# Kernel tuning notes

Measured on AMD Instinct MI355X. Metric: run time of the kernel, lower is better.

The kernel has to match this reference:

```python
import jax, jax.numpy as jnp
import numpy as np

N = 50000      # nodes
E = 500000     # edges per adjacency (avg degree ~10)
IN = 128       # in_dim == hidden_dim so layer weights stack cleanly
HID = 128
C = 40         # n_classes
L = 3          # n_layers
DEG = 10.0


def setup_inputs() -> dict:
    key = jax.random.key(0)
    ks = jax.random.split(key, 14)
    x0 = jax.random.normal(ks[0], (N, IN), jnp.float32)
    # COO sparse adjacency (row-sorted for efficient segment_sum); values mimic mean-normalized weights
    adj_row = jnp.sort(jax.random.randint(ks[1], (E,), 0, N, jnp.int32))
    adj_col = jax.random.randint(ks[2], (E,), 0, N, jnp.int32)
    adj_val = jax.random.uniform(ks[3], (E,), jnp.float32) / DEG
    adj_b_row = jnp.sort(jax.random.randint(ks[4], (E,), 0, N, jnp.int32))
    adj_b_col = jax.random.randint(ks[5], (E,), 0, N, jnp.int32)
    adj_b_val = jax.random.uniform(ks[6], (E,), jnp.float32) / DEG
    id_old_value_new = jax.random.randint(ks[7], (N,), 0, N, jnp.int32)
    mix_ratio = jnp.array([0.5], jnp.float32)
    s = 1.0 / np.sqrt(HID)
    # SAGEConv params: lin_l (applied to aggregated neighbors, carries bias) and lin_r (root)
    Wl = jax.random.uniform(ks[8], (L, HID, HID), jnp.float32, -s, s)
    Wr = jax.random.uniform(ks[9], (L, HID, HID), jnp.float32, -s, s)
    b_sage = jax.random.uniform(ks[10], (L, HID), jnp.float32, -s, s)
    so = 1.0 / np.sqrt(HID)
    W_out = jax.random.uniform(ks[11], (HID, C), jnp.float32, -so, so)
    b_out = jax.random.uniform(ks[12], (C,), jnp.float32, -so, so)
    return dict(x0=x0, adj_row=adj_row, adj_col=adj_col, adj_val=adj_val,
                adj_b_row=adj_b_row, adj_b_col=adj_b_col, adj_b_val=adj_b_val,
                mix_ratio=mix_ratio, id_old_value_new=id_old_value_new,
                Wl=Wl, Wr=Wr, b_sage=b_sage, W_out=W_out, b_out=b_out)


def _sage(x_src, x_dst, row, col, val, Wl_i, Wr_i, b_i):
    # spmm: aggr = adj @ x_src  (gather neighbor feats, scale by edge value, scatter-add to rows)
    msg = x_src[col] * val[:, None]                       # [E, HID]
    aggr = jax.ops.segment_sum(msg, row, num_segments=N)  # [N, HID]
    return aggr @ Wl_i + x_dst @ Wr_i + b_i


def reference(x0, adj_row, adj_col, adj_val, adj_b_row, adj_b_col, adj_b_val,
              mix_ratio, id_old_value_new, Wl, Wr, b_sage, W_out, b_out):
    r = mix_ratio
    # Branch A pre-aggregation stack (dropout is identity in eval mode)
    aggr_xs = [x0]
    x = x0
    for i in range(L - 1):
        x = jax.nn.relu(_sage(x, x, adj_row, adj_col, adj_val, Wl[i], Wr[i], b_sage[i]))
        aggr_xs.append(x)
    # Branch B: gather-based re-indexing of branch-A features
    aggr_xs_b = [h[id_old_value_new] for h in aggr_xs]
    x_mix = aggr_xs[0] * r + aggr_xs_b[0] * (1.0 - r)
    for i in range(L):
        x_new = jax.nn.relu(_sage(aggr_xs[i], x_mix, adj_row, adj_col, adj_val, Wl[i], Wr[i], b_sage[i]))
        x_new_b = jax.nn.relu(_sage(aggr_xs_b[i], x_mix, adj_b_row, adj_b_col, adj_b_val, Wl[i], Wr[i], b_sage[i]))
        x_mix = x_new * r + x_new_b * (1.0 - r)
    logits = x_mix @ W_out + b_out
    return jax.nn.log_softmax(logits, axis=-1)
```

## Files before the change

### kernel.cpp

```cpp
#include <hip/hip_runtime.h>
#include <hip/hip_fp16.h>
#include <math.h>

#define NNODES 50000
#define NEDGES 500000
#define HID 128
#define NCLS 40

using half8v = __attribute__((ext_vector_type(8))) _Float16;
using float4v = __attribute__((ext_vector_type(4))) float;
using uint4v = __attribute__((ext_vector_type(4))) unsigned;

static __device__ __forceinline__ unsigned h2u(__half2 h) {
    union { __half2 h; unsigned u; } x; x.h = h; return x.u;
}
static __device__ __forceinline__ __half2 u2h(unsigned u) {
    union { unsigned u; __half2 h; } x; x.u = u; return x.h;
}

static __device__ __forceinline__ void rowptr_body(const int* __restrict__ row,
                                                   int e, int* __restrict__ rp) {
    if (e >= NEDGES) return;
    int r = row[e];
    int prev = (e == 0) ? -1 : row[e - 1];
    for (int q = prev + 1; q <= r; ++q) rp[q] = e;
    if (e == NEDGES - 1) {
        for (int q = r + 1; q <= NNODES; ++q) rp[q] = NEDGES;
    }
}

static __global__ void prep_edges_kernel(const int* __restrict__ arow,
                                         const int* __restrict__ acol,
                                         const float* __restrict__ aval,
                                         const int* __restrict__ brow,
                                         const int* __restrict__ bcol,
                                         const float* __restrict__ bval,
                                         const int* __restrict__ id,
                                         int* __restrict__ rpa, int* __restrict__ rpb,
                                         int2* __restrict__ cvA, int2* __restrict__ cvB,
                                         int gE) {
    int bid = blockIdx.x;
    if (bid < gE) {
        rowptr_body(arow, bid * 256 + threadIdx.x, rpa);
    } else if (bid < 2 * gE) {
        rowptr_body(brow, (bid - gE) * 256 + threadIdx.x, rpb);
    } else if (bid < 3 * gE) {
        int e = (bid - 2 * gE) * 256 + threadIdx.x;
        if (e < NEDGES) {
            __half2 v = __float2half2_rn(aval[e]);
            cvA[e] = make_int2(acol[e], (int)h2u(v));
        }
    } else {
        int e = (bid - 3 * gE) * 256 + threadIdx.x;
        if (e < NEDGES) {
            __half2 v = __float2half2_rn(bval[e]);
            cvB[e] = make_int2(id[bcol[e]], (int)h2u(v));
        }
    }
}

static __global__ void prep_x_kernel(const float4* __restrict__ x, const int* __restrict__ id,
                                     const float* __restrict__ mixr,
                                     uint2* __restrict__ x0h, uint2* xmh) {
    int i = blockIdx.x * blockDim.x + threadIdx.x;
    int n = i >> 5, qq = i & 31;
    float r = mixr[0];
    float4 a = x[i];
    float4 b = x[(size_t)id[n] * 32 + qq];
    uint2 pa, pm;
    pa.x = h2u(__floats2half2_rn(a.x, a.y));
    pa.y = h2u(__floats2half2_rn(a.z, a.w));
    pm.x = h2u(__floats2half2_rn(r * a.x + (1.f - r) * b.x, r * a.y + (1.f - r) * b.y));
    pm.y = h2u(__floats2half2_rn(r * a.z + (1.f - r) * b.z, r * a.w + (1.f - r) * b.w));
    x0h[i] = pa;
    xmh[i] = pm;
}

static __global__ void prep_w_kernel(const float* __restrict__ Wl, const float* __restrict__ Wr,
                                     const float* __restrict__ Wout,
                                     __half* __restrict__ Wt, __half* __restrict__ WoT) {
    int t = blockIdx.x * blockDim.x + threadIdx.x;
    if (t < 6 * 16384) {
        int mat = t >> 14, idx = t & 16383;
        int n = idx >> 7, k = idx & 127;
        const float* src = (mat < 3) ? (Wl + mat * 16384) : (Wr + (mat - 3) * 16384);
        Wt[t] = __float2half(src[k * HID + n]);
    } else {
        int u = t - 6 * 16384;
        int c = u >> 7, k = u & 127;
        WoT[u] = (c < NCLS) ? __float2half(Wout[k * NCLS + c]) : __float2half(0.f);
    }
}

static __global__ __launch_bounds__(256) void spmm2_kernel(
    const __half* __restrict__ h,
    const int2* __restrict__ cvA, const int* __restrict__ rpA,
    __half* __restrict__ Sh,
    const int2* __restrict__ cvB, const int* __restrict__ rpB,
    __half* __restrict__ Th) {
    int w = blockIdx.x * 4 + (threadIdx.x >> 6);
    const int l = threadIdx.x & 63;
    const int q = l >> 4, j = l & 15;
    const int2* cv; const int* rp; __half* dst; int node;
    if (w < NNODES) { cv = cvA; rp = rpA; dst = Sh; node = w; }
    else            { cv = cvB; rp = rpB; dst = Th; node = w - NNODES; }
    const int e0 = rp[node], e1 = rp[node + 1];
    __half2 a0 = __float2half2_rn(0.f), a1 = a0, a2 = a0, a3 = a0;
    int e = e0 + q;
    int2 m0, m1;
    bool have = (e + 4 < e1);
    if (have) { m0 = cv[e]; m1 = cv[e + 4]; }
    while (have) {
        const int e2 = e + 8;
        const bool nxt = (e2 + 4 < e1);
        int2 k0 = m0, k1 = m1;
        if (nxt) { k0 = cv[e2]; k1 = cv[e2 + 4]; }
        const uint4 p0 = *(const uint4*)(h + (size_t)m0.x * HID + j * 8);
        const uint4 p1 = *(const uint4*)(h + (size_t)m1.x * HID + j * 8);
        const __half2 v0 = u2h((unsigned)m0.y), v1 = u2h((unsigned)m1.y);
        a0 = __hfma2(u2h(p0.x), v0, a0); a1 = __hfma2(u2h(p0.y), v0, a1);
        a2 = __hfma2(u2h(p0.z), v0, a2); a3 = __hfma2(u2h(p0.w), v0, a3);
        a0 = __hfma2(u2h(p1.x), v1, a0); a1 = __hfma2(u2h(p1.y), v1, a1);
        a2 = __hfma2(u2h(p1.z), v1, a2); a3 = __hfma2(u2h(p1.w), v1, a3);
        m0 = k0; m1 = k1; e = e2; have = nxt;
    }
    if (e < e1) {
        const int2 m = cv[e];
        const uint4 p = *(const uint4*)(h + (size_t)m.x * HID + j * 8);
        const __half2 v = u2h((unsigned)m.y);
        a0 = __hfma2(u2h(p.x), v, a0); a1 = __hfma2(u2h(p.y), v, a1);
        a2 = __hfma2(u2h(p.z), v, a2); a3 = __hfma2(u2h(p.w), v, a3);
    }
    a0 = __hadd2(a0, u2h(__shfl_xor((int)h2u(a0), 16)));
    a1 = __hadd2(a1, u2h(__shfl_xor((int)h2u(a1), 16)));
    a2 = __hadd2(a2, u2h(__shfl_xor((int)h2u(a2), 16)));
    a3 = __hadd2(a3, u2h(__shfl_xor((int)h2u(a3), 16)));
    a0 = __hadd2(a0, u2h(__shfl_xor((int)h2u(a0), 32)));
    a1 = __hadd2(a1, u2h(__shfl_xor((int)h2u(a1), 32)));
    a2 = __hadd2(a2, u2h(__shfl_xor((int)h2u(a2), 32)));
    a3 = __hadd2(a3, u2h(__shfl_xor((int)h2u(a3), 32)));
    if (l < 16) {
        uint4v o;
        o.x = h2u(a0); o.y = h2u(a1); o.z = h2u(a2); o.w = h2u(a3);
        __builtin_nontemporal_store(o, (uint4v*)(dst + (size_t)node * HID + l * 8));
    }
}

#define LOAD_H4(ptr, w0, w1, w2, w3)                                            \
    w0 = *(const half8v*)(ptr);                                                 \
    w1 = *(const half8v*)((ptr) + 32);                                          \
    w2 = *(const half8v*)((ptr) + 64);                                          \
    w3 = *(const half8v*)((ptr) + 96);

#define LOAD_H4NT(ptr, w0, w1, w2, w3)                                          \
    w0 = __builtin_nontemporal_load((const half8v*)(ptr));                      \
    w1 = __builtin_nontemporal_load((const half8v*)((ptr) + 32));               \
    w2 = __builtin_nontemporal_load((const half8v*)((ptr) + 64));               \
    w3 = __builtin_nontemporal_load((const half8v*)((ptr) + 96));

#define MFMA4(w0, w1, w2, w3, x0, x1, x2, x3, t)                                \
    t = __builtin_amdgcn_mfma_f32_16x16x32_f16(w0, x0, t, 0, 0, 0);             \
    t = __builtin_amdgcn_mfma_f32_16x16x32_f16(w1, x1, t, 0, 0, 0);             \
    t = __builtin_amdgcn_mfma_f32_16x16x32_f16(w2, x2, t, 0, 0, 0);             \
    t = __builtin_amdgcn_mfma_f32_16x16x32_f16(w3, x3, t, 0, 0, 0);

template <bool DO_HY>
static __global__ __launch_bounds__(64, 2) void fused_layer_kernel(
    const __half* __restrict__ Sh, const __half* __restrict__ Th,
    __half* xm, const __half* __restrict__ hIn,
    const __half* __restrict__ Wl, const __half* __restrict__ Wr,
    const float* __restrict__ bias, const float* __restrict__ mixr,
    __half* __restrict__ hOut,
    const __half* __restrict__ WoT, const float* __restrict__ bout,
    float* __restrict__ out) {
    __shared__ __align__(16) __half hs[16][136];
    const int lr = threadIdx.x & 15;
    const int lg = threadIdx.x >> 4;
    const int row = blockIdx.x * 16 + lr;
    const size_t rbase = (size_t)row * HID;
    const float rr = mixr[0];

    half8v sh0, sh1, sh2, sh3, th0, th1, th2, th3;
    half8v xm0, xm1, xm2, xm3, hh0, hh1, hh2, hh3;
    {
        const __half* p = Sh + rbase + lg * 8;
        LOAD_H4NT(p, sh0, sh1, sh2, sh3)
        p = Th + rbase + lg * 8;
        LOAD_H4NT(p, th0, th1, th2, th3)
        p = xm + rbase + lg * 8;
        LOAD_H4(p, xm0, xm1, xm2, xm3)
        if constexpr (DO_HY) {
            p = hIn + rbase + lg * 8;
            LOAD_H4(p, hh0, hh1, hh2, hh3)
        }
    }
    __builtin_amdgcn_sched_barrier(0);

#pragma unroll
    for (int c = 0; c < 8; ++c) {
        const __half* wlp = Wl + (size_t)(c * 16 + lr) * HID + lg * 8;
        const __half* wrp = Wr + (size_t)(c * 16 + lr) * HID + lg * 8;
        half8v l0, l1, l2, l3, r0, r1, r2, r3;
        LOAD_H4(wlp, l0, l1, l2, l3)
        LOAD_H4(wrp, r0, r1, r2, r3)
        float4v aS = {0.f, 0.f, 0.f, 0.f}, aT = aS, aZ = aS, aH = aS;
        MFMA4(l0, l1, l2, l3, sh0, sh1, sh2, sh3, aS)
        MFMA4(l0, l1, l2, l3, th0, th1, th2, th3, aT)
        MFMA4(r0, r1, r2, r3, xm0, xm1, xm2, xm3, aZ)
        if constexpr (DO_HY) {
            MFMA4(r0, r1, r2, r3, hh0, hh1, hh2, hh3, aH)
        }
        const int col0 = c * 16 + lg * 4;
        const float4v bv = *(const float4v*)(bias + col0);
        __half xm4[4], h4[4];
#pragma unroll
        for (int i = 0; i < 4; ++i) {
            const float z = aZ[i] + bv[i];
            const float xa = fmaxf(aS[i] + z, 0.f);
            const float xb = fmaxf(aT[i] + z, 0.f);
            xm4[i] = __float2half(rr * xa + (1.f - rr) * xb);
            if constexpr (DO_HY) h4[i] = __float2half(fmaxf(aS[i] + aH[i] + bv[i], 0.f));
        }
        uint2 xmv;
        xmv.x = h2u(__half2{xm4[0], xm4[1]});
        xmv.y = h2u(__half2{xm4[2], xm4[3]});
        if constexpr (DO_HY) {
            uint2 hv;
            hv.x = h2u(__half2{h4[0], h4[1]});
            hv.y = h2u(__half2{h4[2], h4[3]});
            *(uint2*)(xm + rbase + col0) = xmv;
            *(uint2*)(hOut + rbase + col0) = hv;
        } else {
            *(uint2*)(&hs[lr][col0]) = xmv;
        }
    }

    if constexpr (!DO_HY) {
        __syncthreads();
        const __half* lp = &hs[lr][lg * 8];
        half8v c0, c1, c2, c3;
        LOAD_H4(lp, c0, c1, c2, c3)
        float lv[3][4];
        float mx = -INFINITY;
#pragma unroll
        for (int c = 0; c < 3; ++c) {
            const __half* wq = WoT + (size_t)(c * 16 + lr) * HID + lg * 8;
            half8v w0, w1, w2, w3;
            LOAD_H4(wq, w0, w1, w2, w3)
            float4v t = {0.f, 0.f, 0.f, 0.f};
            MFMA4(w0, w1, w2, w3, c0, c1, c2, c3, t)
            const int col0 = c * 16 + lg * 4;
            const bool valid = col0 < NCLS;
#pragma unroll
            for (int i = 0; i < 4; ++i) {
                const float l = valid ? (t[i] + bout[col0 + i]) : -INFINITY;
                lv[c][i] = l;
                mx = fmaxf(mx, l);
            }
        }
        mx = fmaxf(mx, __shfl_xor(mx, 16));
        mx = fmaxf(mx, __shfl_xor(mx, 32));
        float sum = 0.f;
#pragma unroll
        for (int c = 0; c < 3; ++c)
#pragma unroll
            for (int i = 0; i < 4; ++i)
                if (lv[c][i] > -INFINITY) sum += expf(lv[c][i] - mx);
        sum += __shfl_xor(sum, 16);
        sum += __shfl_xor(sum, 32);
        const float lse = mx + logf(sum);
#pragma unroll
        for (int c = 0; c < 3; ++c) {
            const int col0 = c * 16 + lg * 4;
            if (col0 < NCLS) {
                float4 o = make_float4(lv[c][0] - lse, lv[c][1] - lse,
                                       lv[c][2] - lse, lv[c][3] - lse);
                *(float4*)(out + (size_t)row * NCLS + col0) = o;
            }
        }
    }
}

extern "C" void kernel_launch(void* const* d_in, const int* in_sizes, int n_in,
                              void* d_out, int out_size, void* d_ws, size_t ws_size,
                              hipStream_t stream) {
    const float* x0   = (const float*)d_in[0];
    const int*   arow = (const int*)d_in[1];
    const int*   acol = (const int*)d_in[2];
    const float* aval = (const float*)d_in[3];
    const int*   brow = (const int*)d_in[4];
    const int*   bcol = (const int*)d_in[5];
    const float* bval = (const float*)d_in[6];
    const float* mixr = (const float*)d_in[7];
    const int*   id   = (const int*)d_in[8];
    const float* Wl   = (const float*)d_in[9];
    const float* Wr   = (const float*)d_in[10];
    const float* bs   = (const float*)d_in[11];
    const float* Wout = (const float*)d_in[12];
    const float* bout = (const float*)d_in[13];
    float* out = (float*)d_out;

    const size_t NF = (size_t)NNODES * HID;
    __half* x0h = (__half*)d_ws;
    __half* xmh = x0h + NF;
    __half* h1  = xmh + NF;
    __half* h2  = h1 + NF;
    __half* Sh  = h2 + NF;
    __half* Th  = Sh + NF;
    __half* Wt  = Th + NF;
    __half* WoT = Wt + 6 * 16384;
    int2* cvA = (int2*)(WoT + 48 * 128);
    int2* cvB = cvA + NEDGES;
    int* rpa = (int*)(cvB + NEDGES);
    int* rpb = rpa + (NNODES + 1);

    const int gE = (NEDGES + 255) / 256;
    const int gC = NNODES * HID / 4 / 256;
    const int gG = NNODES / 16;
    const int gS2 = 2 * NNODES * 64 / 256;

    prep_edges_kernel<<<4 * gE, 256, 0, stream>>>(arow, acol, aval, brow, bcol, bval,
                                                  id, rpa, rpb, cvA, cvB, gE);
    prep_x_kernel<<<gC, 256, 0, stream>>>((const float4*)x0, id, mixr,
                                          (uint2*)x0h, (uint2*)xmh);
    prep_w_kernel<<<(6 * 16384 + 48 * 128) / 256, 256, 0, stream>>>(Wl, Wr, Wout, Wt, WoT);

    spmm2_kernel<<<gS2, 256, 0, stream>>>(x0h, cvA, rpa, Sh, cvB, rpb, Th);
    fused_layer_kernel<true><<<gG, 64, 0, stream>>>(
        Sh, Th, xmh, x0h, Wt + 0 * 16384, Wt + 3 * 16384, bs, mixr,
        h1, nullptr, nullptr, nullptr);

    spmm2_kernel<<<gS2, 256, 0, stream>>>(h1, cvA, rpa, Sh, cvB, rpb, Th);
    fused_layer_kernel<true><<<gG, 64, 0, stream>>>(
        Sh, Th, xmh, h1, Wt + 1 * 16384, Wt + 4 * 16384, bs + 128, mixr,
        h2, nullptr, nullptr, nullptr);

    spmm2_kernel<<<gS2, 256, 0, stream>>>(h2, cvA, rpa, Sh, cvB, rpb, Th);
    fused_layer_kernel<false><<<gG, 64, 0, stream>>>(
        Sh, Th, xmh, nullptr, Wt + 2 * 16384, Wt + 5 * 16384, bs + 256, mixr,
        nullptr, WoT, bout, out);
}
```

Before: 254.3 us.

## Stage layer weights in shared memory shared across four waves per block

The fused dense-layer kernel moves from one 64-thread wave per 16 rows to 256-thread blocks covering 64 rows. Each 16-row chunk of Wl/Wr is loaded cooperatively into double-buffered LDS and read by all four waves, instead of every wave fetching the weights from global/L2 itself. This cuts weight traffic per block, but adds two __syncthreads per chunk iteration and bounds checks for the partial last block.

```diff
diff --git a/kernel.cpp b/kernel.cpp
--- a/kernel.cpp
+++ b/kernel.cpp
@@ -165,7 +165,7 @@
     t = __builtin_amdgcn_mfma_f32_16x16x32_f16(w3, x3, t, 0, 0, 0);
 
 template <bool DO_HY>
-static __global__ __launch_bounds__(64, 2) void fused_layer_kernel(
+static __global__ __launch_bounds__(256, 2) void fused_layer_kernel(
     const __half* __restrict__ Sh, const __half* __restrict__ Th,
     __half* xm, const __half* __restrict__ hIn,
     const __half* __restrict__ Wl, const __half* __restrict__ Wr,
@@ -173,12 +173,18 @@
     __half* __restrict__ hOut,
     const __half* __restrict__ WoT, const float* __restrict__ bout,
     float* __restrict__ out) {
-    __shared__ __align__(16) __half hs[16][136];
-    const int lr = threadIdx.x & 15;
-    const int lg = threadIdx.x >> 4;
-    const int row = blockIdx.x * 16 + lr;
-    const size_t rbase = (size_t)row * HID;
+    __shared__ __align__(16) _Float16 Wls[2][16][136];
+    __shared__ __align__(16) _Float16 Wrs[2][16][136];
+    __shared__ __align__(16) __half hs[DO_HY ? 1 : 64][136];
+    const int tid = threadIdx.x;
+    const int lr = tid & 15;
+    const int lg = (tid >> 4) & 3;
+    const int wv = tid >> 6;
+    const int row = blockIdx.x * 64 + wv * 16 + lr;
+    const int rowc = min(row, NNODES - 1);
+    const size_t rbase = (size_t)rowc * HID;
     const float rr = mixr[0];
+    const int srow = tid >> 4, scol = (tid & 15) * 8;
 
     half8v sh0, sh1, sh2, sh3, th0, th1, th2, th3;
     half8v xm0, xm1, xm2, xm3, hh0, hh1, hh2, hh3;
@@ -194,12 +200,23 @@
             LOAD_H4(p, hh0, hh1, hh2, hh3)
         }
     }
-    __builtin_amdgcn_sched_barrier(0);
+
+    half8v wlreg = *(const half8v*)(Wl + srow * HID + scol);
+    half8v wrreg = *(const half8v*)(Wr + srow * HID + scol);
 
 #pragma unroll
     for (int c = 0; c < 8; ++c) {
-        const __half* wlp = Wl + (size_t)(c * 16 + lr) * HID + lg * 8;
-        const __half* wrp = Wr + (size_t)(c * 16 + lr) * HID + lg * 8;
+        const int buf = c & 1;
+        *(half8v*)&Wls[buf][srow][scol] = wlreg;
+        *(half8v*)&Wrs[buf][srow][scol] = wrreg;
+        if (c < 7) {
+            wlreg = *(const half8v*)(Wl + (c + 1) * 2048 + srow * HID + scol);
+            wrreg = *(const half8v*)(Wr + (c + 1) * 2048 + srow * HID + scol);
+        }
+        __syncthreads();
+
+        const _Float16* wlp = &Wls[buf][lr][lg * 8];
+        const _Float16* wrp = &Wrs[buf][lr][lg * 8];
         half8v l0, l1, l2, l3, r0, r1, r2, r3;
         LOAD_H4(wlp, l0, l1, l2, l3)
         LOAD_H4(wrp, r0, r1, r2, r3)
@@ -228,16 +245,18 @@
             uint2 hv;
             hv.x = h2u(__half2{h4[0], h4[1]});
             hv.y = h2u(__half2{h4[2], h4[3]});
-            *(uint2*)(xm + rbase + col0) = xmv;
-            *(uint2*)(hOut + rbase + col0) = hv;
+            if (row < NNODES) {
+                *(uint2*)(xm + rbase + col0) = xmv;
+                *(uint2*)(hOut + rbase + col0) = hv;
+            }
         } else {
-            *(uint2*)(&hs[lr][col0]) = xmv;
-        }
+            *(uint2*)(&hs[wv * 16 + lr][col0]) = xmv;
+        }
+        __syncthreads();
     }
 
     if constexpr (!DO_HY) {
-        __syncthreads();
-        const __half* lp = &hs[lr][lg * 8];
+        const __half* lp = &hs[wv * 16 + lr][lg * 8];
         half8v c0, c1, c2, c3;
         LOAD_H4(lp, c0, c1, c2, c3)
         float lv[3][4];
@@ -272,7 +291,7 @@
 #pragma unroll
         for (int c = 0; c < 3; ++c) {
             const int col0 = c * 16 + lg * 4;
-            if (col0 < NCLS) {
+            if (col0 < NCLS && row < NNODES) {
                 float4 o = make_float4(lv[c][0] - lse, lv[c][1] - lse,
                                        lv[c][2] - lse, lv[c][3] - lse);
                 *(float4*)(out + (size_t)row * NCLS + col0) = o;
@@ -316,7 +335,7 @@
 
     const int gE = (NEDGES + 255) / 256;
     const int gC = NNODES * HID / 4 / 256;
-    const int gG = NNODES / 16;
+    const int gG = (NNODES + 63) / 64;
     const int gS2 = 2 * NNODES * 64 / 256;
 
     prep_edges_kernel<<<4 * gE, 256, 0, stream>>>(arow, acol, aval, brow, bcol, bval,
@@ -326,17 +345,17 @@
     prep_w_kernel<<<(6 * 16384 + 48 * 128) / 256, 256, 0, stream>>>(Wl, Wr, Wout, Wt, WoT);
 
     spmm2_kernel<<<gS2, 256, 0, stream>>>(x0h, cvA, rpa, Sh, cvB, rpb, Th);
-    fused_layer_kernel<true><<<gG, 64, 0, stream>>>(
+    fused_layer_kernel<true><<<gG, 256, 0, stream>>>(
         Sh, Th, xmh, x0h, Wt + 0 * 16384, Wt + 3 * 16384, bs, mixr,
         h1, nullptr, nullptr, nullptr);
 
     spmm2_kernel<<<gS2, 256, 0, stream>>>(h1, cvA, rpa, Sh, cvB, rpb, Th);
-    fused_layer_kernel<true><<<gG, 64, 0, stream>>>(
+    fused_layer_kernel<true><<<gG, 256, 0, stream>>>(
         Sh, Th, xmh, h1, Wt + 1 * 16384, Wt + 4 * 16384, bs + 128, mixr,
         h2, nullptr, nullptr, nullptr);
 
     spmm2_kernel<<<gS2, 256, 0, stream>>>(h2, cvA, rpa, Sh, cvB, rpb, Th);
-    fused_layer_kernel<false><<<gG, 64, 0, stream>>>(
+    fused_layer_kernel<false><<<gG, 256, 0, stream>>>(
         Sh, Th, xmh, nullptr, Wt + 2 * 16384, Wt + 5 * 16384, bs + 256, mixr,
         nullptr, WoT, bout, out);
 }
```

Measured after the change: 215.8 us. -15.1%, faster.
